# Optimization experiments

Measured on AMD Instinct MI355X. Metric: run time of the kernel, lower is better.

Reference implementation:

```python
import jax, jax.numpy as jnp
import numpy as np

D_MODEL = 256
N_LEVELS = 4
N_HEADS = 8
N_POINTS = 4
D_HEAD = D_MODEL // N_HEADS  # 32
BATCH = 8
SHAPES = np.array([[64, 64], [32, 32], [16, 16], [8, 8]], dtype=np.int32)
LEN_IN = int((SHAPES[:, 0] * SHAPES[:, 1]).sum())  # 5440
LEN_Q = LEN_IN
STARTS = np.concatenate([[0], np.cumsum(SHAPES[:, 0] * SHAPES[:, 1])[:-1]]).astype(np.int32)


def _offset_bias():
    # faithful _reset_parameters grid init for sampling_offsets bias
    thetas = np.arange(N_HEADS, dtype=np.float64) * (2.0 * np.pi / N_HEADS)
    grid = np.stack([np.cos(thetas), np.sin(thetas)], -1)
    grid = grid / np.abs(grid).max(-1, keepdims=True)
    grid = np.tile(grid[:, None, None, :], (1, N_LEVELS, N_POINTS, 1))
    grid = grid * (np.arange(N_POINTS) + 1)[None, None, :, None]
    return jnp.asarray(grid.reshape(-1), dtype=jnp.float32)


def setup_inputs() -> dict:
    key = jax.random.key(0)
    ks = jax.random.split(key, 8)
    s = 1.0 / np.sqrt(D_MODEL)
    return {
        "query": jax.random.normal(ks[0], (BATCH, LEN_Q, D_MODEL), jnp.float32),
        "reference_points": jax.random.uniform(ks[1], (BATCH, LEN_Q, N_LEVELS, 2), jnp.float32),
        "input_flatten": jax.random.normal(ks[2], (BATCH, LEN_IN, D_MODEL), jnp.float32),
        "input_spatial_shapes": jnp.asarray(SHAPES),
        "input_level_start_index": jnp.asarray(STARTS),
        "W_val": jax.random.normal(ks[3], (D_MODEL, D_MODEL), jnp.float32) * s,
        "b_val": jnp.zeros((D_MODEL,), jnp.float32),
        "W_off": jax.random.normal(ks[4], (D_MODEL, N_HEADS * N_LEVELS * N_POINTS * 2), jnp.float32) * 0.01,
        "b_off": _offset_bias(),
        "W_attn": jax.random.normal(ks[5], (D_MODEL, N_HEADS * N_LEVELS * N_POINTS), jnp.float32) * s,
        "b_attn": jnp.zeros((N_HEADS * N_LEVELS * N_POINTS,), jnp.float32),
        "W_out": jax.random.normal(ks[6], (D_MODEL, D_MODEL), jnp.float32) * s,
        "b_out": jnp.zeros((D_MODEL,), jnp.float32),
    }


def _ms_deform_attn_core(value, shapes_np, starts_np, sampling_locations, attention_weights):
    # value: (N, Lin, Hn, d); sampling_locations: (N, Lq, Hn, L, P, 2) in [0,1]
    # attention_weights: (N, Lq, Hn, L, P)
    n, lq = sampling_locations.shape[:2]
    value_t = jnp.transpose(value, (0, 2, 1, 3))  # (N, Hn, Lin, d)
    out = jnp.zeros((n, N_HEADS, lq, value.shape[-1]), value.dtype)
    for lvl in range(N_LEVELS):
        H, W = int(shapes_np[lvl, 0]), int(shapes_np[lvl, 1])
        st = int(starts_np[lvl])
        v = value_t[:, :, st:st + H * W]  # (N, Hn, H*W, d)
        loc = jnp.transpose(sampling_locations[:, :, :, lvl], (0, 2, 1, 3, 4))  # (N, Hn, Lq, P, 2)
        x = loc[..., 0] * W - 0.5
        y = loc[..., 1] * H - 0.5
        x0 = jnp.floor(x).astype(jnp.int32)
        y0 = jnp.floor(y).astype(jnp.int32)
        lx = x - x0
        ly = y - y0
        x1, y1 = x0 + 1, y0 + 1

        def gather(yc, xc):
            valid = (yc >= 0) & (yc < H) & (xc >= 0) & (xc < W)
            idx = jnp.clip(yc, 0, H - 1) * W + jnp.clip(xc, 0, W - 1)
            idx = idx.reshape(n, N_HEADS, -1)  # (N, Hn, Lq*P)
            g = jnp.take_along_axis(v, idx[..., None], axis=2)  # (N, Hn, Lq*P, d)
            return g * valid.reshape(n, N_HEADS, -1, 1)

        w00 = ((1 - lx) * (1 - ly)).reshape(n, N_HEADS, -1, 1)
        w01 = (lx * (1 - ly)).reshape(n, N_HEADS, -1, 1)
        w10 = ((1 - lx) * ly).reshape(n, N_HEADS, -1, 1)
        w11 = (lx * ly).reshape(n, N_HEADS, -1, 1)
        samp = (gather(y0, x0) * w00 + gather(y0, x1) * w01 +
                gather(y1, x0) * w10 + gather(y1, x1) * w11)
        samp = samp.reshape(n, N_HEADS, lq, N_POINTS, -1)
        aw = jnp.transpose(attention_weights[:, :, :, lvl], (0, 2, 1, 3))  # (N, Hn, Lq, P)
        out = out + (samp * aw[..., None]).sum(axis=3)
    return jnp.transpose(out, (0, 2, 1, 3)).reshape(n, lq, -1)


def reference(query, reference_points, input_flatten, input_spatial_shapes,
              input_level_start_index, W_val, b_val, W_off, b_off,
              W_attn, b_attn, W_out, b_out):
    shapes_np = np.asarray(input_spatial_shapes)
    starts_np = np.asarray(input_level_start_index)
    n, lq, _ = query.shape
    lin = input_flatten.shape[1]

    value = (input_flatten @ W_val + b_val).reshape(n, lin, N_HEADS, D_HEAD)
    off = (query @ W_off + b_off).reshape(n, lq, N_HEADS, N_LEVELS, N_POINTS, 2)
    attn = jax.nn.softmax((query @ W_attn + b_attn).reshape(n, lq, N_HEADS, N_LEVELS * N_POINTS), axis=-1)
    attn = attn.reshape(n, lq, N_HEADS, N_LEVELS, N_POINTS)

    # normalizer: (L, 2) as [W, H]
    normalizer = jnp.stack([input_spatial_shapes[:, 1], input_spatial_shapes[:, 0]], -1).astype(query.dtype)
    loc = reference_points[:, :, None, :, None, :] + off / normalizer[None, None, None, :, None, :]

    out = _ms_deform_attn_core(value, shapes_np, starts_np, loc, attn)
    return out @ W_out + b_out
```

## Files before the change

kernel.cpp:

```cpp
#include <hip/hip_runtime.h>

typedef unsigned short ushort;
typedef unsigned int uint;
typedef __bf16 bf16x8 __attribute__((ext_vector_type(8)));
typedef float floatx4 __attribute__((ext_vector_type(4)));
typedef float floatx2 __attribute__((ext_vector_type(2)));
typedef ushort ushort8 __attribute__((ext_vector_type(8)));
typedef uint uintx4 __attribute__((ext_vector_type(4)));

constexpr int LQ = 5440;
constexpr int ROWS = 43520;

__device__ __forceinline__ ushort f2b(float f) {
  union { float f; uint i; } v; v.f = f;
  uint r = v.i + 0x7FFFu + ((v.i >> 16) & 1u);
  return (ushort)(r >> 16);
}
__device__ __forceinline__ float blo(uint u) {
  union { uint i; float f; } v; v.i = u << 16; return v.f;
}
__device__ __forceinline__ float bhi(uint u) {
  union { uint i; float f; } v; v.i = u & 0xFFFF0000u; return v.f;
}

__global__ __launch_bounds__(256) void wcast_kernel(
    const float* __restrict__ Wv, const float* __restrict__ Wo,
    const float* __restrict__ Wa, const float* __restrict__ Wu,
    ushort* __restrict__ Wt) {
  int k = threadIdx.x;
  int n = blockIdx.x;
  int m = blockIdx.y;
  const float* src = (m == 0) ? Wv : (m == 1) ? Wo : (m == 2) ? Wa : Wu;
  int N = (m == 2) ? 128 : 256;
  if (n >= N) return;
  size_t off = (size_t)m * 65536 - ((m == 3) ? 32768 : 0);
  Wt[off + (size_t)n * 256 + k] = f2b(src[(size_t)k * N + n]);
}

template<bool F2B>
__device__ __forceinline__ void tile64_mainloop(
    const void* __restrict__ Av, const ushort* __restrict__ Bt,
    int row_base, int n0, ushort* At, ushort* Bs, floatx4 (&acc)[4][2]) {
  const int t = threadIdx.x;
  const int lane = t & 63, wv = t >> 6;
#pragma unroll
  for (int i = 0; i < 4; ++i)
#pragma unroll
    for (int j = 0; j < 2; ++j) acc[i][j] = floatx4{0.f, 0.f, 0.f, 0.f};

  for (int k0 = 0; k0 < 256; k0 += 32) {
    {
      int r = t >> 2, q = t & 3;
      int slot = ((r >> 4) * 64 + q * 16 + (r & 15)) * 8;
      if (F2B) {
        const float* ap = (const float*)Av + (size_t)(row_base + r) * 256 + k0 + q * 8;
        float4 a0 = *(const float4*)ap, a1 = *(const float4*)(ap + 4);
        ushort8 u;
        u[0] = f2b(a0.x); u[1] = f2b(a0.y); u[2] = f2b(a0.z); u[3] = f2b(a0.w);
        u[4] = f2b(a1.x); u[5] = f2b(a1.y); u[6] = f2b(a1.z); u[7] = f2b(a1.w);
        *(ushort8*)&At[slot] = u;
      } else {
        const ushort* ap = (const ushort*)Av + (size_t)(row_base + r) * 256 + k0 + q * 8;
        *(ushort8*)&At[slot] = *(const ushort8*)ap;
      }
    }
#pragma unroll
    for (int i = 0; i < 2; ++i) {
      int item = t + 256 * i;
      int nr = item >> 2, q = item & 3;
      int slot = ((nr >> 4) * 64 + q * 16 + (nr & 15)) * 8;
      *(ushort8*)&Bs[slot] = *(const ushort8*)(Bt + (size_t)(n0 + nr) * 256 + k0 + q * 8);
    }
    __syncthreads();
    bf16x8 af[4], bf[2];
#pragma unroll
    for (int ti = 0; ti < 4; ++ti)
      af[ti] = *(const bf16x8*)&At[(ti * 64 + lane) * 8];
#pragma unroll
    for (int tjj = 0; tjj < 2; ++tjj)
      bf[tjj] = *(const bf16x8*)&Bs[((2 * wv + tjj) * 64 + lane) * 8];
#pragma unroll
    for (int ti = 0; ti < 4; ++ti)
#pragma unroll
      for (int tjj = 0; tjj < 2; ++tjj)
        acc[ti][tjj] = __builtin_amdgcn_mfma_f32_16x16x32_bf16(af[ti], bf[tjj], acc[ti][tjj], 0, 0, 0);
    __syncthreads();
  }
}

__global__ __launch_bounds__(256) void gemm_val64(
    const float* __restrict__ X, const ushort* __restrict__ WtV,
    const float* __restrict__ bval, ushort* __restrict__ value16) {
  __shared__ ushort At[2048];
  __shared__ ushort Bs[4096];
  floatx4 acc[4][2];
  int row_base = blockIdx.x * 64, n0 = blockIdx.y * 128;
  tile64_mainloop<true>(X, WtV, row_base, n0, At, Bs, acc);
  const int t = threadIdx.x, lane = t & 63, wv = t >> 6;
  const int quad = lane >> 4, l15 = lane & 15;
#pragma unroll
  for (int tjj = 0; tjj < 2; ++tjj) {
    int gcol = n0 + (2 * wv + tjj) * 16 + l15;
    float b = bval[gcol];
#pragma unroll
    for (int ti = 0; ti < 4; ++ti)
#pragma unroll
      for (int reg = 0; reg < 4; ++reg) {
        int grow = row_base + ti * 16 + quad * 4 + reg;
        value16[(size_t)grow * 256 + gcol] = f2b(acc[ti][tjj][reg] + b);
      }
  }
}

__global__ __launch_bounds__(256) void gemm_oa_kernel(
    const float* __restrict__ Q, const ushort* __restrict__ WtOA,
    const float* __restrict__ boff, const float* __restrict__ battn,
    const float* __restrict__ refp, uint4* __restrict__ tblq) {
  __shared__ ushort At[2048];
  __shared__ ushort Bs[3072];
  const int t = threadIdx.x;
  const int lane = t & 63, wv = t >> 6;
  const int quad = lane >> 4, l15 = lane & 15;
  const int bx = blockIdx.x;
  const int row_base = (bx % 680) * 64;
  const int hp = bx / 680;
  floatx4 accO[4], accA[2];
#pragma unroll
  for (int p = 0; p < 4; ++p) accO[p] = floatx4{0.f, 0.f, 0.f, 0.f};
#pragma unroll
  for (int q = 0; q < 2; ++q) accA[q] = floatx4{0.f, 0.f, 0.f, 0.f};

  for (int k0 = 0; k0 < 256; k0 += 32) {
    {
      int r = t >> 2, q = t & 3;
      const float* ap = Q + (size_t)(row_base + r) * 256 + k0 + q * 8;
      float4 a0 = *(const float4*)ap, a1 = *(const float4*)(ap + 4);
      ushort8 u;
      u[0] = f2b(a0.x); u[1] = f2b(a0.y); u[2] = f2b(a0.z); u[3] = f2b(a0.w);
      u[4] = f2b(a1.x); u[5] = f2b(a1.y); u[6] = f2b(a1.z); u[7] = f2b(a1.w);
      *(ushort8*)&At[((r >> 4) * 64 + q * 16 + (r & 15)) * 8] = u;
    }
#pragma unroll
    for (int i = 0; i < 2; ++i) {
      int item = t + 256 * i;
      if (item < 384) {
        int nrl = item >> 2, q = item & 3;
        int grow_ = (nrl < 64) ? (hp * 64 + nrl) : (256 + hp * 32 + (nrl - 64));
        *(ushort8*)&Bs[((nrl >> 4) * 64 + q * 16 + (nrl & 15)) * 8] =
            *(const ushort8*)(WtOA + (size_t)grow_ * 256 + k0 + q * 8);
      }
    }
    __syncthreads();
    bf16x8 af = *(const bf16x8*)&At[(wv * 64 + lane) * 8];
#pragma unroll
    for (int p = 0; p < 4; ++p) {
      bf16x8 bf = *(const bf16x8*)&Bs[(p * 64 + lane) * 8];
      accO[p] = __builtin_amdgcn_mfma_f32_16x16x32_bf16(af, bf, accO[p], 0, 0, 0);
    }
#pragma unroll
    for (int q = 0; q < 2; ++q) {
      bf16x8 bf = *(const bf16x8*)&Bs[((4 + q) * 64 + lane) * 8];
      accA[q] = __builtin_amdgcn_mfma_f32_16x16x32_bf16(af, bf, accA[q], 0, 0, 0);
    }
    __syncthreads();
  }

  const int lp = l15, l = lp >> 2;
  const int wd = 64 >> l;
  const int st = (l == 0) ? 0 : (l == 1) ? 4096 : (l == 2) ? 5120 : 5376;
  const float lw = (float)wd;
  const int src = (quad << 4) | (2 * (lp & 7));
  float boO[4], boA[2];
#pragma unroll
  for (int p = 0; p < 4; ++p) boO[p] = boff[(4 * hp + p) * 16 + l15];
#pragma unroll
  for (int q = 0; q < 2; ++q) boA[q] = battn[(2 * hp + q) * 16 + l15];

#pragma unroll
  for (int reg = 0; reg < 4; ++reg) {
    int grow = row_base + wv * 16 + quad * 4 + reg;
    float rx = refp[(size_t)grow * 8 + l * 2];
    float ry = refp[(size_t)grow * 8 + l * 2 + 1];
#pragma unroll
    for (int hh = 0; hh < 2; ++hh) {
      int h = 2 * hp + hh;
      float xa = accA[hh][reg] + boA[hh];
      float m = xa;
      m = fmaxf(m, __shfl_xor(m, 1, 64));
      m = fmaxf(m, __shfl_xor(m, 2, 64));
      m = fmaxf(m, __shfl_xor(m, 4, 64));
      m = fmaxf(m, __shfl_xor(m, 8, 64));
      float e = __expf(xa - m);
      float ssum = e;
      ssum += __shfl_xor(ssum, 1, 64);
      ssum += __shfl_xor(ssum, 2, 64);
      ssum += __shfl_xor(ssum, 4, 64);
      ssum += __shfl_xor(ssum, 8, 64);
      float aw = e / ssum;
      float v0 = accO[2 * hh][reg] + boO[2 * hh];
      float v1 = accO[2 * hh + 1][reg] + boO[2 * hh + 1];
      float x_lo = __shfl(v0, src, 64),     x_hi = __shfl(v1, src, 64);
      float y_lo = __shfl(v0, src | 1, 64), y_hi = __shfl(v1, src | 1, 64);
      float xo = (lp < 8) ? x_lo : x_hi;
      float yo = (lp < 8) ? y_lo : y_hi;
      float X = rx * lw + xo - 0.5f;
      float Y = ry * lw + yo - 0.5f;
      float fx = floorf(X), fy = floorf(Y);
      float lx = X - fx, ly = Y - fy;
      int x0 = (int)fx, y0 = (int)fy, x1 = x0 + 1, y1 = y0 + 1;
      int cx0 = min(max(x0, 0), wd - 1), cx1 = min(max(x1, 0), wd - 1);
      int cy0 = min(max(y0, 0), wd - 1), cy1 = min(max(y1, 0), wd - 1);
      float vx0 = (x0 >= 0 && x0 < wd) ? 1.f : 0.f;
      float vx1 = (x1 >= 0 && x1 < wd) ? 1.f : 0.f;
      float vy0 = (y0 >= 0 && y0 < wd) ? 1.f : 0.f;
      float vy1 = (y1 >= 0 && y1 < wd) ? 1.f : 0.f;
      float g00 = (1.f - lx) * (1.f - ly) * vx0 * vy0 * aw;
      float g01 = lx * (1.f - ly) * vx1 * vy0 * aw;
      float g10 = (1.f - lx) * ly * vx0 * vy1 * aw;
      float g11 = lx * ly * vx1 * vy1 * aw;
      uint i00 = st + cy0 * wd + cx0, i01 = st + cy0 * wd + cx1;
      uint i10 = st + cy1 * wd + cx0, i11 = st + cy1 * wd + cx1;
      uint4 ov;
      ov.x = i00 | (i01 << 16);
      ov.y = i10 | (i11 << 16);
      ov.z = (uint)f2b(g00) | ((uint)f2b(g01) << 16);
      ov.w = (uint)f2b(g10) | ((uint)f2b(g11) << 16);
      tblq[((size_t)grow * 8 + h) * 16 + lp] = ov;
    }
  }
}

__global__ __launch_bounds__(512) void core_kernel(
    const ushort* __restrict__ value16, const uint4* __restrict__ tblq,
    uint* __restrict__ coreo32) {
  const int bx = blockIdx.x;
  const int b = bx & 7;
  const int pr = bx >> 3;
  const int brow0 = b * LQ + pr * 2;
  const int t = threadIdx.x;
  const int h = t >> 6, lane = t & 63;
  const int s = lane >> 3, g = lane & 7;
  const size_t sb = ((size_t)brow0 * 8 + h) * 16;

  const uintx4* tb = (const uintx4*)tblq;
  uintx4 s0 = __builtin_nontemporal_load(tb + sb + s);
  uintx4 s1 = __builtin_nontemporal_load(tb + sb + 8 + s);
  uintx4 s2 = __builtin_nontemporal_load(tb + sb + 128 + s);
  uintx4 s3 = __builtin_nontemporal_load(tb + sb + 136 + s);

  const char* vb = (const char*)value16 + (uint)(b * (LQ * 512) + (h << 6));
  const uint g8 = (uint)(g << 3);

  uint2 v[16];
#define GL(d, idx16) d = *(const uint2*)(vb + (((idx16) << 9) + g8))
  GL(v[0],  (s0[0] & 0xFFFFu)); GL(v[1],  (s0[0] >> 16));
  GL(v[2],  (s0[1] & 0xFFFFu)); GL(v[3],  (s0[1] >> 16));
  GL(v[4],  (s1[0] & 0xFFFFu)); GL(v[5],  (s1[0] >> 16));
  GL(v[6],  (s1[1] & 0xFFFFu)); GL(v[7],  (s1[1] >> 16));
  GL(v[8],  (s2[0] & 0xFFFFu)); GL(v[9],  (s2[0] >> 16));
  GL(v[10], (s2[1] & 0xFFFFu)); GL(v[11], (s2[1] >> 16));
  GL(v[12], (s3[0] & 0xFFFFu)); GL(v[13], (s3[0] >> 16));
  GL(v[14], (s3[1] & 0xFFFFu)); GL(v[15], (s3[1] >> 16));
#undef GL

  floatx2 a01 = {0.f, 0.f}, a23 = {0.f, 0.f};
  floatx2 c01 = {0.f, 0.f}, c23 = {0.f, 0.f};

  auto accum4 = [&](uint wz, uint ww, const uint2* vv, floatx2& x01, floatx2& x23) {
    const float ws[4] = {blo(wz), bhi(wz), blo(ww), bhi(ww)};
#pragma unroll
    for (int j = 0; j < 4; ++j) {
      floatx2 wj = {ws[j], ws[j]};
      floatx2 p = {blo(vv[j].x), bhi(vv[j].x)};
      floatx2 q = {blo(vv[j].y), bhi(vv[j].y)};
      x01 = __builtin_elementwise_fma(wj, p, x01);
      x23 = __builtin_elementwise_fma(wj, q, x23);
    }
  };
  accum4(s0[2], s0[3], &v[0],  a01, a23);
  accum4(s1[2], s1[3], &v[4],  a01, a23);
  accum4(s2[2], s2[3], &v[8],  c01, c23);
  accum4(s3[2], s3[3], &v[12], c01, c23);

#pragma unroll
  for (int m = 8; m <= 32; m <<= 1) {
    a01.x += __shfl_xor(a01.x, m, 64);
    a01.y += __shfl_xor(a01.y, m, 64);
    a23.x += __shfl_xor(a23.x, m, 64);
    a23.y += __shfl_xor(a23.y, m, 64);
    c01.x += __shfl_xor(c01.x, m, 64);
    c01.y += __shfl_xor(c01.y, m, 64);
    c23.x += __shfl_xor(c23.x, m, 64);
    c23.y += __shfl_xor(c23.y, m, 64);
  }
  if (s == 0) {
    uint2 o0, o1;
    o0.x = (uint)f2b(a01.x) | ((uint)f2b(a01.y) << 16);
    o0.y = (uint)f2b(a23.x) | ((uint)f2b(a23.y) << 16);
    o1.x = (uint)f2b(c01.x) | ((uint)f2b(c01.y) << 16);
    o1.y = (uint)f2b(c23.x) | ((uint)f2b(c23.y) << 16);
    *(uint2*)(coreo32 + (size_t)brow0 * 128 + h * 16 + g * 2) = o0;
    *(uint2*)(coreo32 + (size_t)(brow0 + 1) * 128 + h * 16 + g * 2) = o1;
  }
}

__global__ __launch_bounds__(256) void gemm_out64(
    const ushort* __restrict__ C, const ushort* __restrict__ WtU,
    const float* __restrict__ bout, float* __restrict__ out) {
  __shared__ ushort At[2048];
  __shared__ ushort Bs[4096];
  floatx4 acc[4][2];
  int row_base = blockIdx.x * 64, n0 = blockIdx.y * 128;
  tile64_mainloop<false>(C, WtU, row_base, n0, At, Bs, acc);
  const int t = threadIdx.x, lane = t & 63, wv = t >> 6;
  const int quad = lane >> 4, l15 = lane & 15;
#pragma unroll
  for (int tjj = 0; tjj < 2; ++tjj) {
    int gcol = n0 + (2 * wv + tjj) * 16 + l15;
    float b = bout[gcol];
#pragma unroll
    for (int ti = 0; ti < 4; ++ti)
#pragma unroll
      for (int reg = 0; reg < 4; ++reg) {
        int grow = row_base + ti * 16 + quad * 4 + reg;
        out[(size_t)grow * 256 + gcol] = acc[ti][tjj][reg] + b;
      }
  }
}

extern "C" void kernel_launch(void* const* d_in, const int* in_sizes, int n_in,
                              void* d_out, int out_size, void* d_ws, size_t ws_size,
                              hipStream_t stream) {
  const float* query  = (const float*)d_in[0];
  const float* refp   = (const float*)d_in[1];
  const float* inpf   = (const float*)d_in[2];
  const float* W_val  = (const float*)d_in[5];
  const float* b_val  = (const float*)d_in[6];
  const float* W_off  = (const float*)d_in[7];
  const float* b_off  = (const float*)d_in[8];
  const float* W_attn = (const float*)d_in[9];
  const float* b_attn = (const float*)d_in[10];
  const float* W_out  = (const float*)d_in[11];
  const float* b_out  = (const float*)d_in[12];

  char* ws = (char*)d_ws;
  ushort* Wt    = (ushort*)ws;
  ushort* value = (ushort*)(ws + 1048576);
  uint4*  tbl   = (uint4*)(ws + 23330816);
  ushort* coreo = (ushort*)(ws + 112459776);

  dim3 blk(256);
  wcast_kernel<<<dim3(256, 4), blk, 0, stream>>>(W_val, W_off, W_attn, W_out, Wt);
  gemm_val64  <<<dim3(680, 2), blk, 0, stream>>>(inpf, Wt, b_val, value);
  gemm_oa_kernel<<<dim3(2720), blk, 0, stream>>>(query, Wt + 65536, b_off, b_attn, refp, tbl);
  core_kernel <<<dim3(21760), dim3(512), 0, stream>>>(value, tbl, (uint*)coreo);
  gemm_out64  <<<dim3(680, 2), blk, 0, stream>>>(coreo, Wt + 163840, b_out, (float*)d_out);
}
```

Before: 333.4 us.

## Stage coarse-level value rows in LDS for core sampling kernel

```diff
diff --git a/kernel.cpp b/kernel.cpp
--- a/kernel.cpp
+++ b/kernel.cpp
@@ -230,77 +230,101 @@
   }
 }
 
-__global__ __launch_bounds__(512) void core_kernel(
+__global__ __launch_bounds__(1024) void core_kernel(
     const ushort* __restrict__ value16, const uint4* __restrict__ tblq,
     uint* __restrict__ coreo32) {
+  extern __shared__ char lds[];
   const int bx = blockIdx.x;
   const int b = bx & 7;
-  const int pr = bx >> 3;
-  const int brow0 = b * LQ + pr * 2;
+  const int tile = bx >> 3;
   const int t = threadIdx.x;
-  const int h = t >> 6, lane = t & 63;
+
+  {
+    const char* src = (const char*)value16 + ((size_t)b * 5440 + 5120) * 512;
+#pragma unroll
+    for (int i = 0; i < 10; ++i) {
+      int u = t + (i << 10);
+      int row = u >> 5, c = u & 31;
+      uint4 d = *(const uint4*)(src + (size_t)u * 16);
+      *(uint4*)(lds + row * 512 + ((c ^ ((row & 7) << 2)) << 4)) = d;
+    }
+  }
+  __syncthreads();
+
+  const int w = t >> 6, lane = t & 63;
   const int s = lane >> 3, g = lane & 7;
-  const size_t sb = ((size_t)brow0 * 8 + h) * 16;
-
+  const uint g8 = (uint)(g << 3);
+  const char* vbase = (const char*)value16 + (size_t)b * (LQ * 512);
   const uintx4* tb = (const uintx4*)tblq;
-  uintx4 s0 = __builtin_nontemporal_load(tb + sb + s);
-  uintx4 s1 = __builtin_nontemporal_load(tb + sb + 8 + s);
-  uintx4 s2 = __builtin_nontemporal_load(tb + sb + 128 + s);
-  uintx4 s3 = __builtin_nontemporal_load(tb + sb + 136 + s);
-
-  const char* vb = (const char*)value16 + (uint)(b * (LQ * 512) + (h << 6));
-  const uint g8 = (uint)(g << 3);
-
-  uint2 v[16];
-#define GL(d, idx16) d = *(const uint2*)(vb + (((idx16) << 9) + g8))
-  GL(v[0],  (s0[0] & 0xFFFFu)); GL(v[1],  (s0[0] >> 16));
-  GL(v[2],  (s0[1] & 0xFFFFu)); GL(v[3],  (s0[1] >> 16));
-  GL(v[4],  (s1[0] & 0xFFFFu)); GL(v[5],  (s1[0] >> 16));
-  GL(v[6],  (s1[1] & 0xFFFFu)); GL(v[7],  (s1[1] >> 16));
-  GL(v[8],  (s2[0] & 0xFFFFu)); GL(v[9],  (s2[0] >> 16));
-  GL(v[10], (s2[1] & 0xFFFFu)); GL(v[11], (s2[1] >> 16));
-  GL(v[12], (s3[0] & 0xFFFFu)); GL(v[13], (s3[0] >> 16));
-  GL(v[14], (s3[1] & 0xFFFFu)); GL(v[15], (s3[1] >> 16));
-#undef GL
-
-  floatx2 a01 = {0.f, 0.f}, a23 = {0.f, 0.f};
-  floatx2 c01 = {0.f, 0.f}, c23 = {0.f, 0.f};
-
-  auto accum4 = [&](uint wz, uint ww, const uint2* vv, floatx2& x01, floatx2& x23) {
-    const float ws[4] = {blo(wz), bhi(wz), blo(ww), bhi(ww)};
-#pragma unroll
-    for (int j = 0; j < 4; ++j) {
-      floatx2 wj = {ws[j], ws[j]};
-      floatx2 p = {blo(vv[j].x), bhi(vv[j].x)};
-      floatx2 q = {blo(vv[j].y), bhi(vv[j].y)};
-      x01 = __builtin_elementwise_fma(wj, p, x01);
-      x23 = __builtin_elementwise_fma(wj, q, x23);
-    }
-  };
-  accum4(s0[2], s0[3], &v[0],  a01, a23);
-  accum4(s1[2], s1[3], &v[4],  a01, a23);
-  accum4(s2[2], s2[3], &v[8],  c01, c23);
-  accum4(s3[2], s3[3], &v[12], c01, c23);
-
-#pragma unroll
-  for (int m = 8; m <= 32; m <<= 1) {
-    a01.x += __shfl_xor(a01.x, m, 64);
-    a01.y += __shfl_xor(a01.y, m, 64);
-    a23.x += __shfl_xor(a23.x, m, 64);
-    a23.y += __shfl_xor(a23.y, m, 64);
-    c01.x += __shfl_xor(c01.x, m, 64);
-    c01.y += __shfl_xor(c01.y, m, 64);
-    c23.x += __shfl_xor(c23.x, m, 64);
-    c23.y += __shfl_xor(c23.y, m, 64);
-  }
-  if (s == 0) {
-    uint2 o0, o1;
-    o0.x = (uint)f2b(a01.x) | ((uint)f2b(a01.y) << 16);
-    o0.y = (uint)f2b(a23.x) | ((uint)f2b(a23.y) << 16);
-    o1.x = (uint)f2b(c01.x) | ((uint)f2b(c01.y) << 16);
-    o1.y = (uint)f2b(c23.x) | ((uint)f2b(c23.y) << 16);
-    *(uint2*)(coreo32 + (size_t)brow0 * 128 + h * 16 + g * 2) = o0;
-    *(uint2*)(coreo32 + (size_t)(brow0 + 1) * 128 + h * 16 + g * 2) = o1;
+  const int bq = b * LQ + tile * 16;
+
+  for (int it = 0; it < 4; ++it) {
+    const int combo = (it << 4) + w;
+    const int h = combo & 7;
+    const int pr = combo >> 3;
+    const int brow0 = bq + pr * 2;
+    const size_t sb = ((size_t)brow0 * 8 + h) * 16;
+
+    uintx4 s0 = __builtin_nontemporal_load(tb + sb + s);
+    uintx4 s1 = __builtin_nontemporal_load(tb + sb + 8 + s);
+    uintx4 s2 = __builtin_nontemporal_load(tb + sb + 128 + s);
+    uintx4 s3 = __builtin_nontemporal_load(tb + sb + 136 + s);
+
+    const char* vbh = vbase + (h << 6);
+    uint2 va[8];
+#define GLO(d, idx16) d = *(const uint2*)(vbh + (((uint)(idx16) << 9) + g8))
+    GLO(va[0], (s0[0] & 0xFFFFu)); GLO(va[1], (s0[0] >> 16));
+    GLO(va[2], (s0[1] & 0xFFFFu)); GLO(va[3], (s0[1] >> 16));
+    GLO(va[4], (s2[0] & 0xFFFFu)); GLO(va[5], (s2[0] >> 16));
+    GLO(va[6], (s2[1] & 0xFFFFu)); GLO(va[7], (s2[1] >> 16));
+#undef GLO
+    uint2 vl[8];
+#define LDO(d, idx16) { uint r_ = (uint)(idx16) - 5120u; \
+    d = *(const uint2*)(lds + (r_ << 9) + (((uint)h ^ (r_ & 7u)) << 6) + g8); }
+    LDO(vl[0], (s1[0] & 0xFFFFu)); LDO(vl[1], (s1[0] >> 16));
+    LDO(vl[2], (s1[1] & 0xFFFFu)); LDO(vl[3], (s1[1] >> 16));
+    LDO(vl[4], (s3[0] & 0xFFFFu)); LDO(vl[5], (s3[0] >> 16));
+    LDO(vl[6], (s3[1] & 0xFFFFu)); LDO(vl[7], (s3[1] >> 16));
+#undef LDO
+
+    floatx2 a01 = {0.f, 0.f}, a23 = {0.f, 0.f};
+    floatx2 c01 = {0.f, 0.f}, c23 = {0.f, 0.f};
+    auto accum4 = [&](uint wz, uint ww, const uint2* vv, floatx2& x01, floatx2& x23) {
+      const float ws[4] = {blo(wz), bhi(wz), blo(ww), bhi(ww)};
+#pragma unroll
+      for (int j = 0; j < 4; ++j) {
+        floatx2 wj = {ws[j], ws[j]};
+        floatx2 p = {blo(vv[j].x), bhi(vv[j].x)};
+        floatx2 q = {blo(vv[j].y), bhi(vv[j].y)};
+        x01 = __builtin_elementwise_fma(wj, p, x01);
+        x23 = __builtin_elementwise_fma(wj, q, x23);
+      }
+    };
+    accum4(s0[2], s0[3], &va[0], a01, a23);
+    accum4(s1[2], s1[3], &vl[0], a01, a23);
+    accum4(s2[2], s2[3], &va[4], c01, c23);
+    accum4(s3[2], s3[3], &vl[4], c01, c23);
+
+#pragma unroll
+    for (int m = 8; m <= 32; m <<= 1) {
+      a01.x += __shfl_xor(a01.x, m, 64);
+      a01.y += __shfl_xor(a01.y, m, 64);
+      a23.x += __shfl_xor(a23.x, m, 64);
+      a23.y += __shfl_xor(a23.y, m, 64);
+      c01.x += __shfl_xor(c01.x, m, 64);
+      c01.y += __shfl_xor(c01.y, m, 64);
+      c23.x += __shfl_xor(c23.x, m, 64);
+      c23.y += __shfl_xor(c23.y, m, 64);
+    }
+    if (s == 0) {
+      uint2 o0, o1;
+      o0.x = (uint)f2b(a01.x) | ((uint)f2b(a01.y) << 16);
+      o0.y = (uint)f2b(a23.x) | ((uint)f2b(a23.y) << 16);
+      o1.x = (uint)f2b(c01.x) | ((uint)f2b(c01.y) << 16);
+      o1.y = (uint)f2b(c23.x) | ((uint)f2b(c23.y) << 16);
+      *(uint2*)(coreo32 + (size_t)brow0 * 128 + h * 16 + g * 2) = o0;
+      *(uint2*)(coreo32 + (size_t)(brow0 + 1) * 128 + h * 16 + g * 2) = o1;
+    }
   }
 }
 
@@ -349,10 +373,17 @@
   uint4*  tbl   = (uint4*)(ws + 23330816);
   ushort* coreo = (ushort*)(ws + 112459776);
 
+  static bool attr_set = false;
+  if (!attr_set) {
+    hipFuncSetAttribute((const void*)core_kernel,
+                        hipFuncAttributeMaxDynamicSharedMemorySize, 163840);
+    attr_set = true;
+  }
+
   dim3 blk(256);
   wcast_kernel<<<dim3(256, 4), blk, 0, stream>>>(W_val, W_off, W_attn, W_out, Wt);
   gemm_val64  <<<dim3(680, 2), blk, 0, stream>>>(inpf, Wt, b_val, value);
   gemm_oa_kernel<<<dim3(2720), blk, 0, stream>>>(query, Wt + 65536, b_off, b_attn, refp, tbl);
-  core_kernel <<<dim3(21760), dim3(512), 0, stream>>>(value, tbl, (uint*)coreo);
+  core_kernel <<<dim3(2720), dim3(1024), 163840, stream>>>(value, tbl, (uint*)coreo);
   gemm_out64  <<<dim3(680, 2), blk, 0, stream>>>(coreo, Wt + 163840, b_out, (float*)d_out);
 }
```

Measured after the change: 339.4 us. About the same (+1.8%).
